# Optimization experiments

Hardware: AMD Instinct MI355X
Metric: run time of the kernel (lower is better)

## Reference

```python
import jax, jax.numpy as jnp
import numpy as np

N_NODES = 1024   # 'num_edges' arg of the torch module (used as node count)
DEG = 16         # ring connectivity -> symmetric directed edge set
D = 8            # stalk_dim
EPS_DIAG = 1e-5
EPS_EIG = 1e-6


def setup_inputs() -> dict:
    key = jax.random.key(0)
    n, d = N_NODES, D
    base = jnp.arange(n)
    # undirected ring-chord edges (i, i+k mod n), k=1..DEG, then add reverses
    dst_half = jnp.concatenate([(base + k) % n for k in range(1, DEG + 1)])
    src_half = jnp.tile(base, DEG)
    src = jnp.concatenate([src_half, dst_half]).astype(jnp.int32)
    dst = jnp.concatenate([dst_half, src_half]).astype(jnp.int32)
    e_half = n * DEG
    rev = jnp.concatenate([jnp.arange(e_half) + e_half,
                           jnp.arange(e_half)]).astype(jnp.int32)
    maps = jax.random.normal(key, (2 * e_half, d, d), dtype=jnp.float32) * 0.3
    return {"maps": maps, "src": src, "dst": dst, "rev": rev, "n": n}


def reference(maps, src, dst, rev, n):
    d = maps.shape[-1]
    # diagonal blocks: sum over edges e=(v,u) of F_vu^T F_vu, grouped by v
    ftf = jnp.einsum('eka,ekb->eab', maps, maps)              # (E,d,d)
    diag = jax.ops.segment_sum(ftf, src, num_segments=n)      # (n,d,d)
    # off-diagonal block at (v,u): -F_uv^T @ F_vu (reverse edge always exists)
    off = -jnp.einsum('eka,ekb->eab', maps[rev], maps)        # (E,d,d)
    # assemble dense block Laplacian LF as (n,d,n,d)
    LF4 = jnp.zeros((n, d, n, d), dtype=maps.dtype)
    idx = jnp.arange(n)
    LF4 = LF4.at[idx, :, idx, :].set(diag)
    LF4 = LF4.at[src, :, dst, :].set(off)
    # per-node D_v^{-1/2} via batched eigh
    Dv = diag + EPS_DIAG * jnp.eye(d, dtype=maps.dtype)       # (n,d,d)
    w, V = jnp.linalg.eigh(Dv)
    w_inv_sqrt = 1.0 / jnp.sqrt(jnp.maximum(w, EPS_EIG))      # (n,d)
    Dinv = jnp.einsum('nab,nb,ncb->nac', V, w_inv_sqrt, V)    # (n,d,d)
    # Delta_F = D^{-1/2} LF D^{-1/2} (block-diagonal D -> per-block scaling)
    Delta = jnp.einsum('vab,vbuc,ucd->vaud', Dinv, LF4, Dinv)
    return Delta.reshape(n * d, n * d)
```

## Files before the change

### kernel.cpp

```cpp
#include <hip/hip_runtime.h>


#define NS_ITERS 18

__global__ __launch_bounds__(256) void node_prep_kernel(
    const float* __restrict__ maps, float* __restrict__ diagbuf,
    float* __restrict__ dinv, int n, int deg) {
  __shared__ float F[4][64], Y[4][64], Z[4][64], W[4][64];
  const int g = threadIdx.x >> 6, t = threadIdx.x & 63;
  const int i = t >> 3, j = t & 7;
  const int v = blockIdx.x * 4 + g;
  const int e_half = n * deg;

  float acc = 0.f;
  for (int s = 0; s < 2 * deg; ++s) {
    int e;
    if (s < deg) {
      e = s * n + v;
    } else {
      const int k = s - deg;
      int u = v - k - 1;
      if (u < 0) u += n;
      e = e_half + k * n + u;
    }
    F[g][t] = maps[(size_t)e * 64 + t];
    __syncthreads();
#pragma unroll
    for (int k = 0; k < 8; ++k) acc += F[g][k * 8 + i] * F[g][k * 8 + j];
    __syncthreads();
  }
  diagbuf[(size_t)v * 64 + t] = acc;

  const float a = acc + ((i == j) ? 1e-5f : 0.f);
  Y[g][t] = a;
  __syncthreads();
  float c = 0.f;
#pragma unroll
  for (int k = 0; k < 8; ++k) c += Y[g][k * 8 + k];
  const float rc = 1.f / c;
  __syncthreads();
  Y[g][t] = a * rc;
  Z[g][t] = (i == j) ? 1.f : 0.f;
  __syncthreads();
  for (int it = 0; it < NS_ITERS; ++it) {
    float tr = 0.f;
#pragma unroll
    for (int k = 0; k < 8; ++k) tr += Z[g][i * 8 + k] * Y[g][k * 8 + j];
    const float w = 0.5f * (((i == j) ? 3.f : 0.f) - tr);
    W[g][t] = w;
    __syncthreads();
    float yn = 0.f, zn = 0.f;
#pragma unroll
    for (int k = 0; k < 8; ++k) {
      yn += Y[g][i * 8 + k] * W[g][k * 8 + j];
      zn += W[g][i * 8 + k] * Z[g][k * 8 + j];
    }
    __syncthreads();
    Y[g][t] = yn;
    Z[g][t] = zn;
    __syncthreads();
  }
  dinv[(size_t)v * 64 + t] = Z[g][t] * rsqrtf(c);
}

__global__ __launch_bounds__(256) void row_fill_kernel(
    const float* __restrict__ maps, const float* __restrict__ diagbuf,
    const float* __restrict__ dinv, float* __restrict__ out, int n, int deg) {
  __shared__ float4 blk4[33 * 16];
  float* blk = (float*)blk4;
  __shared__ float DV[64], AV[64];
  __shared__ float FE[4][64], FR[4][64], DU[4][64], TT[4][64];
  __shared__ unsigned char lut[1024];

  const int tid = threadIdx.x;
  const int g = tid >> 6, t = tid & 63;
  const int i = t >> 3, j = t & 7;
  const int v = blockIdx.x;
  const int e_half = n * deg;

  for (int c = tid; c < n; c += 256) lut[c] = 0xFF;
  if (tid < 64) {
    DV[t] = dinv[(size_t)v * 64 + t];
    AV[t] = diagbuf[(size_t)v * 64 + t];
  }
  if (tid == 0) lut[v] = 0;
  __syncthreads();

  if (tid < 64) {
    float s1 = 0.f;
#pragma unroll
    for (int k = 0; k < 8; ++k) s1 += AV[i * 8 + k] * DV[k * 8 + j];
    TT[0][t] = s1;
  }
  __syncthreads();
  if (tid < 64) {
    float b = 0.f;
#pragma unroll
    for (int k = 0; k < 8; ++k) b += DV[i * 8 + k] * TT[0][k * 8 + j];
    blk[t] = b;
  }
  __syncthreads();

  const int per = (2 * deg) / 4;
  for (int it = 0; it < per; ++it) {
    const int s = g * per + it;
    int e, u, r;
    if (s < deg) {
      e = s * n + v;
      u = v + s + 1;
      if (u >= n) u -= n;
      r = e + e_half;
    } else {
      const int k = s - deg;
      u = v - k - 1;
      if (u < 0) u += n;
      e = e_half + k * n + u;
      r = e - e_half;
    }
    FE[g][t] = maps[(size_t)e * 64 + t];
    FR[g][t] = maps[(size_t)r * 64 + t];
    DU[g][t] = dinv[(size_t)u * 64 + t];
    if (t == 0) lut[u] = (unsigned char)(s + 1);
    __syncthreads();
    float o = 0.f;
#pragma unroll
    for (int k = 0; k < 8; ++k) o += FR[g][k * 8 + i] * FE[g][k * 8 + j];
    TT[g][t] = -o;
    __syncthreads();
    float t1 = 0.f;
#pragma unroll
    for (int k = 0; k < 8; ++k) t1 += TT[g][i * 8 + k] * DU[g][k * 8 + j];
    __syncthreads();
    TT[g][t] = t1;
    __syncthreads();
    float b = 0.f;
#pragma unroll
    for (int k = 0; k < 8; ++k) b += DV[i * 8 + k] * TT[g][k * 8 + j];
    blk[(s + 1) * 64 + t] = b;
    __syncthreads();
  }

  const int row4 = n * 2;
  float4* out4 = (float4*)out;
  const float4 zero4 = make_float4(0.f, 0.f, 0.f, 0.f);
  size_t rowbase = (size_t)v * 8 * row4;
  for (int ri = 0; ri < 8; ++ri, rowbase += row4) {
    for (int c4 = tid; c4 < row4; c4 += 256) {
      const int c8 = c4 >> 1, h = c4 & 1;
      const unsigned char sl = lut[c8];
      float4 val = zero4;
      if (sl != 0xFF) val = blk4[(int)sl * 16 + ri * 2 + h];
      out4[rowbase + c4] = val;
    }
  }
}

extern "C" void kernel_launch(void* const* d_in, const int* in_sizes, int n_in,
                              void* d_out, int out_size, void* d_ws,
                              size_t ws_size, hipStream_t stream) {
  const float* maps = (const float*)d_in[0];
  float* out = (float*)d_out;

  const int E = in_sizes[1];
  const int n = E / 32;
  const int deg = E / (2 * n);

  float* diagbuf = (float*)d_ws;
  float* dinv = diagbuf + (size_t)n * 64;

  node_prep_kernel<<<n / 4, 256, 0, stream>>>(maps, diagbuf, dinv, n, deg);
  row_fill_kernel<<<n, 256, 0, stream>>>(maps, diagbuf, dinv, out, n, deg);
}
```

Baseline: 307.6 us.

## Batch edge loads up front, reorder block matmuls, and use nontemporal output stores

node_prep now loads all 32 incident edge maps with vectorized float4 loads into shared memory before a single barrier, replacing a per-edge load/sync loop. row_fill also preloads all 8 edges per group, then computes the off-diagonal block as Dv*(-F_rev^T)*F_e*Du, so each edge needs two barriers instead of four, and the diagonal block is folded into the first iteration. The dense zero-filled output rows are written with nontemporal stores and a 2x unrolled loop to ease cache pressure on the large streaming write. Shared memory per block grows substantially, which may reduce occupancy.

```diff
diff --git a/kernel.cpp b/kernel.cpp
--- a/kernel.cpp
+++ b/kernel.cpp
@@ -3,17 +3,22 @@
 
 #define NS_ITERS 18
 
+typedef float vf4 __attribute__((ext_vector_type(4)));
+
 __global__ __launch_bounds__(256) void node_prep_kernel(
     const float* __restrict__ maps, float* __restrict__ diagbuf,
     float* __restrict__ dinv, int n, int deg) {
-  __shared__ float F[4][64], Y[4][64], Z[4][64], W[4][64];
+  __shared__ float F[4][32][64];
+  __shared__ float Y[4][64], Z[4][64], W[4][64];
   const int g = threadIdx.x >> 6, t = threadIdx.x & 63;
   const int i = t >> 3, j = t & 7;
   const int v = blockIdx.x * 4 + g;
   const int e_half = n * deg;
+  const int q = t >> 4, f4 = t & 15;
 
-  float acc = 0.f;
-  for (int s = 0; s < 2 * deg; ++s) {
+#pragma unroll
+  for (int p = 0; p < 8; ++p) {
+    const int s = p * 4 + q;
     int e;
     if (s < deg) {
       e = s * n + v;
@@ -23,11 +28,15 @@
       if (u < 0) u += n;
       e = e_half + k * n + u;
     }
-    F[g][t] = maps[(size_t)e * 64 + t];
-    __syncthreads();
+    const vf4 val = ((const vf4*)(maps + (size_t)e * 64))[f4];
+    ((vf4*)F[g][s])[f4] = val;
+  }
+  __syncthreads();
+
+  float acc = 0.f;
+  for (int s = 0; s < 32; ++s) {
 #pragma unroll
-    for (int k = 0; k < 8; ++k) acc += F[g][k * 8 + i] * F[g][k * 8 + j];
-    __syncthreads();
+    for (int k = 0; k < 8; ++k) acc += F[g][s][k * 8 + i] * F[g][s][k * 8 + j];
   }
   diagbuf[(size_t)v * 64 + t] = acc;
 
@@ -66,10 +75,10 @@
 __global__ __launch_bounds__(256) void row_fill_kernel(
     const float* __restrict__ maps, const float* __restrict__ diagbuf,
     const float* __restrict__ dinv, float* __restrict__ out, int n, int deg) {
-  __shared__ float4 blk4[33 * 16];
-  float* blk = (float*)blk4;
-  __shared__ float DV[64], AV[64];
-  __shared__ float FE[4][64], FR[4][64], DU[4][64], TT[4][64];
+  __shared__ float blk[33 * 64];
+  __shared__ float FE[4][8][64], FR[4][8][64], DU[4][8][64];
+  __shared__ float TTa[4][64], TTb[4][64];
+  __shared__ float DV[64], AV[64], DT[64];
   __shared__ unsigned char lut[1024];
 
   const int tid = threadIdx.x;
@@ -84,26 +93,10 @@
     AV[t] = diagbuf[(size_t)v * 64 + t];
   }
   if (tid == 0) lut[v] = 0;
-  __syncthreads();
 
-  if (tid < 64) {
-    float s1 = 0.f;
 #pragma unroll
-    for (int k = 0; k < 8; ++k) s1 += AV[i * 8 + k] * DV[k * 8 + j];
-    TT[0][t] = s1;
-  }
-  __syncthreads();
-  if (tid < 64) {
-    float b = 0.f;
-#pragma unroll
-    for (int k = 0; k < 8; ++k) b += DV[i * 8 + k] * TT[0][k * 8 + j];
-    blk[t] = b;
-  }
-  __syncthreads();
-
-  const int per = (2 * deg) / 4;
-  for (int it = 0; it < per; ++it) {
-    const int s = g * per + it;
+  for (int it = 0; it < 8; ++it) {
+    const int s = g * 8 + it;
     int e, u, r;
     if (s < deg) {
       e = s * n + v;
@@ -117,40 +110,56 @@
       e = e_half + k * n + u;
       r = e - e_half;
     }
-    FE[g][t] = maps[(size_t)e * 64 + t];
-    FR[g][t] = maps[(size_t)r * 64 + t];
-    DU[g][t] = dinv[(size_t)u * 64 + t];
+    FE[g][it][t] = maps[(size_t)e * 64 + t];
+    FR[g][it][t] = maps[(size_t)r * 64 + t];
+    DU[g][it][t] = dinv[(size_t)u * 64 + t];
     if (t == 0) lut[u] = (unsigned char)(s + 1);
+  }
+  __syncthreads();
+
+  for (int it = 0; it < 8; ++it) {
+    float qv = 0.f;
+#pragma unroll
+    for (int k = 0; k < 8; ++k) qv += DV[i * 8 + k] * FR[g][it][j * 8 + k];
+    TTa[g][t] = -qv;
+    if (it == 0 && tid < 64) {
+      float s1 = 0.f;
+#pragma unroll
+      for (int k = 0; k < 8; ++k) s1 += AV[i * 8 + k] * DV[k * 8 + j];
+      DT[t] = s1;
+    }
     __syncthreads();
-    float o = 0.f;
+    float pv = 0.f;
 #pragma unroll
-    for (int k = 0; k < 8; ++k) o += FR[g][k * 8 + i] * FE[g][k * 8 + j];
-    TT[g][t] = -o;
-    __syncthreads();
-    float t1 = 0.f;
+    for (int k = 0; k < 8; ++k) pv += TTa[g][i * 8 + k] * FE[g][it][k * 8 + j];
+    TTb[g][t] = pv;
+    if (it == 0 && tid < 64) {
+      float b0 = 0.f;
 #pragma unroll
-    for (int k = 0; k < 8; ++k) t1 += TT[g][i * 8 + k] * DU[g][k * 8 + j];
-    __syncthreads();
-    TT[g][t] = t1;
+      for (int k = 0; k < 8; ++k) b0 += DV[i * 8 + k] * DT[k * 8 + j];
+      blk[t] = b0;
+    }
     __syncthreads();
     float b = 0.f;
 #pragma unroll
-    for (int k = 0; k < 8; ++k) b += DV[i * 8 + k] * TT[g][k * 8 + j];
-    blk[(s + 1) * 64 + t] = b;
-    __syncthreads();
+    for (int k = 0; k < 8; ++k) b += TTb[g][i * 8 + k] * DU[g][it][k * 8 + j];
+    blk[(g * 8 + it + 1) * 64 + t] = b;
   }
+  __syncthreads();
 
   const int row4 = n * 2;
-  float4* out4 = (float4*)out;
-  const float4 zero4 = make_float4(0.f, 0.f, 0.f, 0.f);
+  vf4* out4 = (vf4*)out;
+  const vf4* blk4 = (const vf4*)blk;
+  const vf4 zero4 = {0.f, 0.f, 0.f, 0.f};
   size_t rowbase = (size_t)v * 8 * row4;
   for (int ri = 0; ri < 8; ++ri, rowbase += row4) {
+#pragma unroll 2
     for (int c4 = tid; c4 < row4; c4 += 256) {
       const int c8 = c4 >> 1, h = c4 & 1;
       const unsigned char sl = lut[c8];
-      float4 val = zero4;
+      vf4 val = zero4;
       if (sl != 0xFF) val = blk4[(int)sl * 16 + ri * 2 + h];
-      out4[rowbase + c4] = val;
+      __builtin_nontemporal_store(val, &out4[rowbase + c4]);
     }
   }
 }
```

Measured after the change: 300.2 us. -2.4%, faster.
